# Performance work log

Measured on AMD Instinct MI355X. Metric: run time of the kernel, lower is better.

## Reference

```python
import jax, jax.numpy as jnp
import numpy as np

NEG_SLOPE = 0.2  # PyG GATv2 leaky_relu slope
LN_EPS = 1e-5


def _layernorm(x, gamma, beta):
    mu = x.mean(-1, keepdims=True)
    var = x.var(-1, keepdims=True)
    return (x - mu) * jax.lax.rsqrt(var + LN_EPS) * gamma + beta


def _gatv2_conv(x, src, dst, eattr, Wl, Wr, We, att, bias, concat):
    """PyG GATv2Conv (eval mode). x:(N,F), src/dst:(E,), eattr:(E,edge_dim), att:(H,C)."""
    N = x.shape[0]
    H, C = att.shape
    xl = (x @ Wl).reshape(N, H, C)   # source transform (messages)
    xr = (x @ Wr).reshape(N, H, C)   # target transform
    e = (eattr @ We).reshape(-1, H, C)
    m = xl[src] + xr[dst] + e                                   # (E,H,C)
    score = jnp.sum(jax.nn.leaky_relu(m, NEG_SLOPE) * att, -1)  # (E,H)
    # segment softmax over incoming edges per destination node
    smax = jax.ops.segment_max(score, dst, num_segments=N)
    ex = jnp.exp(score - smax[dst])
    denom = jax.ops.segment_sum(ex, dst, num_segments=N)
    alpha = ex / (denom[dst] + 1e-16)                           # (E,H)
    out = jax.ops.segment_sum(alpha[:, :, None] * xl[src], dst, num_segments=N)  # (N,H,C)
    out = out.reshape(N, H * C) if concat else out.mean(axis=1)
    return out + bias


def setup_inputs() -> dict:
    key = jax.random.key(0)
    ks = jax.random.split(key, 20)
    N, E = 10000, 320000
    D, HID, HEADS, ED = 256, 128, 4, 4
    HC = HID * HEADS  # 512

    def w(k, fi, fo):
        return jax.random.normal(k, (fi, fo), jnp.float32) / np.sqrt(fi)

    x = jax.random.normal(ks[0], (N, D), jnp.float32)
    edge_index = jax.random.randint(ks[1], (2, E), 0, N, jnp.int64)
    edge_attr = jax.random.normal(ks[2], (E, ED), jnp.float32)
    return {
        "x": x, "edge_index": edge_index, "edge_attr": edge_attr,
        # layer 1: heads=4, concat=True
        "Wl1": w(ks[3], D, HC), "Wr1": w(ks[4], D, HC), "We1": w(ks[5], ED, HC),
        "att1": jax.random.normal(ks[6], (HEADS, HID), jnp.float32) / np.sqrt(HID),
        "b1": jnp.zeros((HC,), jnp.float32),
        "g1": jnp.ones((HC,), jnp.float32), "be1": jnp.zeros((HC,), jnp.float32),
        # layer 2: heads=1, concat=False
        "Wl2": w(ks[7], HC, D), "Wr2": w(ks[8], HC, D), "We2": w(ks[9], ED, D),
        "att2": jax.random.normal(ks[10], (1, D), jnp.float32) / np.sqrt(D),
        "b2": jnp.zeros((D,), jnp.float32),
        "g2": jnp.ones((D,), jnp.float32), "be2": jnp.zeros((D,), jnp.float32),
    }


def reference(x, edge_index, edge_attr,
              Wl1, Wr1, We1, att1, b1, g1, be1,
              Wl2, Wr2, We2, att2, b2, g2, be2):
    N = x.shape[0]
    # PyG default add_self_loops=True with edge_attr fill_value='mean'
    loop = jnp.arange(N, dtype=edge_index.dtype)
    src = jnp.concatenate([edge_index[0], loop])
    dst = jnp.concatenate([edge_index[1], loop])
    ea = jnp.concatenate([edge_attr, jnp.broadcast_to(edge_attr.mean(0), (N, edge_attr.shape[1]))])

    h = _gatv2_conv(x, src, dst, ea, Wl1, Wr1, We1, att1, b1, concat=True)
    h = _layernorm(h, g1, be1)
    h = jax.nn.elu(h)  # dropout is identity in eval mode

    h = _gatv2_conv(h, src, dst, ea, Wl2, Wr2, We2, att2, b2, concat=False)
    h = _layernorm(h, g2, be2)
    return h + x  # residual (in_channels == out_channels)
```

## Files before the change

### kernel.cpp

```cpp
#include <hip/hip_runtime.h>
#include <hip/hip_bf16.h>

#define HC1 512
#define HC2 256
#define D_IN 256

typedef __hip_bfloat16  bf16;
typedef __hip_bfloat162 bf162;
typedef __attribute__((ext_vector_type(8))) short short8;
typedef __attribute__((ext_vector_type(4))) float f32x4;
typedef __attribute__((ext_vector_type(2))) float f32x2;

__device__ __forceinline__ void unpack8p(short8 q, f32x2* xa) {
  union { short8 s; unsigned u[4]; } uu; uu.s = q;
#pragma unroll
  for (int j = 0; j < 4; j++) {
    union { unsigned u; float f; } lo, hi;
    lo.u = uu.u[j] << 16;
    hi.u = uu.u[j] & 0xffff0000u;
    xa[j].x = lo.f; xa[j].y = hi.f;
  }
}
__device__ __forceinline__ void load8p(const float* p, f32x2* d) {
  float4 a = *(const float4*)p, b = *(const float4*)(p + 4);
  d[0].x = a.x; d[0].y = a.y; d[1].x = a.z; d[1].y = a.w;
  d[2].x = b.x; d[2].y = b.y; d[3].x = b.z; d[3].y = b.w;
}

template <int CTRL>
__device__ __forceinline__ float dppadd(float x) {
  union { float f; int i; } u, v;
  u.f = x;
  v.i = __builtin_amdgcn_update_dpp(0, u.i, CTRL, 0xF, 0xF, true);
  return x + v.f;
}
__device__ __forceinline__ float red16(float p) {
  p = dppadd<0xB1>(p);
  p = dppadd<0x4E>(p);
  p = dppadd<0x124>(p);
  p = dppadd<0x128>(p);
  return p;
}

__device__ __forceinline__ void glds16(const bf16* g, bf16* l) {
#if __has_builtin(__builtin_amdgcn_global_load_lds)
  __builtin_amdgcn_global_load_lds(
      (const __attribute__((address_space(1))) void*)g,
      (__attribute__((address_space(3))) void*)l, 16, 0, 0);
#else
  int lane = threadIdx.x & 63;
  ((int4*)l)[lane] = *(const int4*)g;
#endif
}

__global__ __launch_bounds__(256)
void gemm_mfma_kernel(const bf16* __restrict__ A, const bf16* __restrict__ BT,
                      bf16* __restrict__ C, int M, int K, int N) {
  __shared__ bf16 lds[8192];
  const int t = threadIdx.x;
  const int w  = t >> 6, l = t & 63;
  const int wr = w >> 1, wc = w & 1;
  const int lo = l & 15, hi = l >> 4;
  const int m0 = blockIdx.y * 128;
  const int n0 = blockIdx.x * 128;

  f32x4 acc[4][4] = {};

  const int c0 = w * 2, c1 = w * 2 + 1;
  const int kc0 = c0 >> 1, r0 = (c0 & 1) * 64 + l;
  const int kc1 = c1 >> 1, r1 = (c1 & 1) * 64 + l;
  int mr0 = m0 + r0; if (mr0 >= M) mr0 = M - 1;
  int mr1 = m0 + r1; if (mr1 >= M) mr1 = M - 1;
  const bf16* ga0 = A + (size_t)mr0 * K + kc0 * 8;
  const bf16* ga1 = A + (size_t)mr1 * K + kc1 * 8;
  const bf16* gb0 = BT + (size_t)(n0 + r0) * K + kc0 * 8;
  const bf16* gb1 = BT + (size_t)(n0 + r1) * K + kc1 * 8;
  bf16* la0 = &lds[c0 * 512];
  bf16* la1 = &lds[c1 * 512];
  bf16* lb0 = &lds[4096 + c0 * 512];
  bf16* lb1 = &lds[4096 + c1 * 512];

  for (int k0 = 0; k0 < K; k0 += 32) {
    if (k0) __syncthreads();
    glds16(ga0 + k0, la0);
    glds16(ga1 + k0, la1);
    glds16(gb0 + k0, lb0);
    glds16(gb1 + k0, lb1);
    __syncthreads();

    short8 af[4], bfr[4];
#pragma unroll
    for (int f = 0; f < 4; f++) {
      af[f]  = *(const short8*)&lds[hi * 1024 + (wr * 64 + f * 16 + lo) * 8];
      bfr[f] = *(const short8*)&lds[4096 + hi * 1024 + (wc * 64 + f * 16 + lo) * 8];
    }
#pragma unroll
    for (int fm = 0; fm < 4; fm++)
#pragma unroll
      for (int fn = 0; fn < 4; fn++)
        acc[fm][fn] = __builtin_amdgcn_mfma_f32_16x16x32_bf16(af[fm], bfr[fn],
                                                              acc[fm][fn], 0, 0, 0);
  }

#pragma unroll
  for (int fm = 0; fm < 4; fm++) {
#pragma unroll
    for (int r = 0; r < 4; r++) {
      int row = m0 + wr * 64 + fm * 16 + hi * 4 + r;
      if (row < M) {
#pragma unroll
        for (int fn = 0; fn < 4; fn++) {
          int col = n0 + wc * 64 + fn * 16 + lo;
          C[(size_t)row * N + col] = __float2bfloat16(acc[fm][fn][r]);
        }
      }
    }
  }
}

__global__ void convx_kernel(const float* __restrict__ x, bf16* __restrict__ xb, int n4) {
  int i = blockIdx.x * blockDim.x + threadIdx.x;
  if (i >= n4) return;
  float4 v = ((const float4*)x)[i];
  union { bf16 h[4]; uint2 u; } cv;
  cv.h[0] = __float2bfloat16(v.x); cv.h[1] = __float2bfloat16(v.y);
  cv.h[2] = __float2bfloat16(v.z); cv.h[3] = __float2bfloat16(v.w);
  ((uint2*)xb)[i] = cv.u;
}

__global__ __launch_bounds__(256)
void transw_kernel(const float* __restrict__ Wl1, const float* __restrict__ Wr1,
                   const float* __restrict__ Wl2, const float* __restrict__ Wr2,
                   bf16* __restrict__ W1T, bf16* __restrict__ W2T) {
  __shared__ float tile[32][33];
  const int z = blockIdx.z;
  const float* in; bf16* out; int K, Nn;
  if (z == 0)      { in = Wl1; out = W1T;             K = 256; Nn = 512; }
  else if (z == 1) { in = Wr1; out = W1T + 512 * 256; K = 256; Nn = 512; }
  else if (z == 2) { in = Wl2; out = W2T;             K = 512; Nn = 256; }
  else             { in = Wr2; out = W2T + 256 * 512; K = 512; Nn = 256; }
  const int nt = blockIdx.x * 32, kt = blockIdx.y * 32;
  if (nt >= Nn || kt >= K) return;
  const int tx = threadIdx.x & 31, ty = threadIdx.x >> 5;
#pragma unroll
  for (int j = 0; j < 4; j++)
    tile[ty + j * 8][tx] = in[(size_t)(kt + ty + j * 8) * Nn + nt + tx];
  __syncthreads();
#pragma unroll
  for (int j = 0; j < 4; j++)
    out[(size_t)(nt + ty + j * 8) * K + kt + tx] = __float2bfloat16(tile[tx][ty + j * 8]);
}

__global__ void mean_kernel(const float* __restrict__ eattr, float* __restrict__ sums, int E) {
  int tid = blockIdx.x * blockDim.x + threadIdx.x;
  int stride = gridDim.x * blockDim.x;
  float l0 = 0.f, l1 = 0.f, l2 = 0.f, l3 = 0.f;
  for (int e = tid; e < E; e += stride) {
    float4 v = ((const float4*)eattr)[e];
    l0 += v.x; l1 += v.y; l2 += v.z; l3 += v.w;
  }
#pragma unroll
  for (int o = 1; o < 64; o <<= 1) {
    l0 += __shfl_xor(l0, o); l1 += __shfl_xor(l1, o);
    l2 += __shfl_xor(l2, o); l3 += __shfl_xor(l3, o);
  }
  if ((threadIdx.x & 63) == 0) {
    atomicAdd(&sums[0], l0); atomicAdd(&sums[1], l1);
    atomicAdd(&sums[2], l2); atomicAdd(&sums[3], l3);
  }
}

__global__ void meanw_kernel(const float* __restrict__ sums, float* __restrict__ mean4, float invE) {
  int t = threadIdx.x;
  if (t < 4) mean4[t] = sums[t] * invE;
}

__global__ void count_kernel(const int* __restrict__ ei, int* __restrict__ counts, int E, int Etot) {
  int tid = blockIdx.x * blockDim.x + threadIdx.x;
  int stride = gridDim.x * blockDim.x;
  for (int e = tid; e < Etot; e += stride) {
    int dst = (e < E) ? ei[E + e] : (e - E);
    atomicAdd(&counts[dst], 1);
  }
}

__global__ __launch_bounds__(1024)
void scan_kernel(const int* __restrict__ counts, int* __restrict__ offs, int N) {
  __shared__ int wsum[16];
  int tid = threadIdx.x, wid = tid >> 6, lane = tid & 63;
  if (tid == 0) offs[0] = 0;
  int carry = 0;
  for (int base = 0; base < N; base += 1024) {
    int i = base + tid;
    int v = (i < N) ? counts[i] : 0;
    int s = v;
#pragma unroll
    for (int o = 1; o < 64; o <<= 1) {
      int u = __shfl_up(s, o);
      if (lane >= o) s += u;
    }
    if (lane == 63) wsum[wid] = s;
    __syncthreads();
    if (wid == 0) {
      int t2 = (lane < 16) ? wsum[lane] : 0;
#pragma unroll
      for (int o = 1; o < 16; o <<= 1) {
        int u = __shfl_up(t2, o);
        if (lane >= o) t2 += u;
      }
      if (lane < 16) wsum[lane] = t2;
    }
    __syncthreads();
    int pre = (wid > 0) ? wsum[wid - 1] : 0;
    int tot = wsum[15];
    if (i < N) offs[i + 1] = carry + pre + s;
    carry += tot;
    __syncthreads();
  }
}

__global__ void fill_kernel(const int* __restrict__ ei, const int* __restrict__ offs,
                            int* __restrict__ cursor, const float* __restrict__ eattr,
                            const float* __restrict__ mean4, int* __restrict__ srcs,
                            float4* __restrict__ eaC, int E, int Etot) {
  int tid = blockIdx.x * blockDim.x + threadIdx.x;
  int stride = gridDim.x * blockDim.x;
  for (int e = tid; e < Etot; e += stride) {
    int src, dst;
    if (e < E) { src = ei[e]; dst = ei[E + e]; } else { src = e - E; dst = src; }
    int pos = atomicAdd(&cursor[dst], 1);
    int slot = offs[dst] + pos;
    srcs[slot] = src;
    eaC[slot] = (e < E) ? ((const float4*)eattr)[e] : *(const float4*)mean4;
  }
}

__global__ __launch_bounds__(256, 3)
void fused1_kernel(const int* __restrict__ srcs, const float4* __restrict__ eaC,
                   const int* __restrict__ offs, const bf16* __restrict__ xlr,
                   const float* __restrict__ We, const float* __restrict__ att,
                   const float* __restrict__ bias, const float* __restrict__ g,
                   const float* __restrict__ be, bf16* __restrict__ h1) {
  const int v = blockIdx.x;
  const int tid = threadIdx.x;
  const int wave = tid >> 6, lane = tid & 63;
  const int ch = lane * 8;

  f32x2 w0p[4], w1p[4], w2p[4], w3p[4], awp[4], xrp[4];
  load8p(We + 0 * HC1 + ch, w0p);
  load8p(We + 1 * HC1 + ch, w1p);
  load8p(We + 2 * HC1 + ch, w2p);
  load8p(We + 3 * HC1 + ch, w3p);
  load8p(att + ch, awp);
  unpack8p(*(const short8*)(xlr + (size_t)v * 1024 + 512 + ch), xrp);

  const int beg = offs[v], end = offs[v + 1];
  const int len = end - beg;
  const int chunk = (len + 3) >> 2;
  int ib = beg + wave * chunk;
  int ie = ib + chunk;
  if (ib > end) ib = end;
  if (ie > end) ie = end;

  float den = 0.f;
  f32x2 accp[4] = {};

  auto edge = [&](short8 q, float4 e) {
    f32x2 xa[4]; unpack8p(q, xa);
    f32x2 p2 = {0.f, 0.f};
#pragma unroll
    for (int j = 0; j < 4; j++) {
      f32x2 m = xa[j] + xrp[j];
      m += e.x * w0p[j];
      m += e.y * w1p[j];
      m += e.z * w2p[j];
      m += e.w * w3p[j];
      f32x2 lm = __builtin_elementwise_max(m, m * 0.2f);
      p2 += lm * awp[j];
    }
    float p = p2.x + p2.y;
    p = red16(p);
    float ex = __expf(p);
    den += ex;
#pragma unroll
    for (int j = 0; j < 4; j++) accp[j] += xa[j] * ex;
  };

  int i = ib;
  if (i + 4 <= ie) {
    int s0 = srcs[i], s1 = srcs[i + 1], s2 = srcs[i + 2], s3 = srcs[i + 3];
    float4 e0 = eaC[i], e1 = eaC[i + 1], e2 = eaC[i + 2], e3 = eaC[i + 3];
    short8 q0 = *(const short8*)(xlr + (size_t)s0 * 1024 + ch);
    short8 q1 = *(const short8*)(xlr + (size_t)s1 * 1024 + ch);
    short8 q2 = *(const short8*)(xlr + (size_t)s2 * 1024 + ch);
    short8 q3 = *(const short8*)(xlr + (size_t)s3 * 1024 + ch);
    i += 4;
    for (; i + 4 <= ie; i += 4) {
      int t0 = srcs[i], t1 = srcs[i + 1], t2 = srcs[i + 2], t3 = srcs[i + 3];
      short8 r0 = *(const short8*)(xlr + (size_t)t0 * 1024 + ch);
      short8 r1 = *(const short8*)(xlr + (size_t)t1 * 1024 + ch);
      short8 r2 = *(const short8*)(xlr + (size_t)t2 * 1024 + ch);
      short8 r3 = *(const short8*)(xlr + (size_t)t3 * 1024 + ch);
      edge(q0, e0); edge(q1, e1); edge(q2, e2); edge(q3, e3);
      e0 = eaC[i]; e1 = eaC[i + 1]; e2 = eaC[i + 2]; e3 = eaC[i + 3];
      q0 = r0; q1 = r1; q2 = r2; q3 = r3;
    }
    edge(q0, e0); edge(q1, e1); edge(q2, e2); edge(q3, e3);
  }
  for (; i < ie; ++i) {
    int s0 = srcs[i];
    float4 e0 = eaC[i];
    short8 q0 = *(const short8*)(xlr + (size_t)s0 * 1024 + ch);
    edge(q0, e0);
  }

  __shared__ float accs[4][HC1];
  __shared__ float dens[4][4];
  __shared__ float2 red[4];
  *(float4*)&accs[wave][ch]     = *(float4*)&accp[0];
  *(float4*)&accs[wave][ch + 4] = *(float4*)&accp[2];
  if ((lane & 15) == 0) dens[wave][lane >> 4] = den;
  __syncthreads();

  const int c = tid * 2;
  const int head = c >> 7;
  const float dtot = dens[0][head] + dens[1][head] + dens[2][head] + dens[3][head];
  const float rden = 1.f / (dtot + 1e-16f);
  float2 a0 = *(float2*)&accs[0][c];
  float2 a1 = *(float2*)&accs[1][c];
  float2 a2 = *(float2*)&accs[2][c];
  float2 a3 = *(float2*)&accs[3][c];
  float2 bv = *(const float2*)(bias + c);
  float val0 = (a0.x + a1.x + a2.x + a3.x) * rden + bv.x;
  float val1 = (a0.y + a1.y + a2.y + a3.y) * rden + bv.y;

  float s1 = val0 + val1, s2 = val0 * val0 + val1 * val1;
  s1 = red16(s1); s2 = red16(s2);
  s1 += __shfl_xor(s1, 16); s2 += __shfl_xor(s2, 16);
  s1 += __shfl_xor(s1, 32); s2 += __shfl_xor(s2, 32);
  if (lane == 0) red[wave] = make_float2(s1, s2);
  __syncthreads();
  float ts1 = red[0].x + red[1].x + red[2].x + red[3].x;
  float ts2 = red[0].y + red[1].y + red[2].y + red[3].y;
  float mu  = ts1 * (1.f / HC1);
  float var = ts2 * (1.f / HC1) - mu * mu;
  float rs  = rsqrtf(var + 1e-5f);

  float2 gv = *(const float2*)(g + c);
  float2 ev = *(const float2*)(be + c);
  float ya = (val0 - mu) * rs * gv.x + ev.x;
  float yb = (val1 - mu) * rs * gv.y + ev.y;
  ya = (ya > 0.f) ? ya : expm1f(ya);
  yb = (yb > 0.f) ? yb : expm1f(yb);
  bf162 hv;
  hv.x = __float2bfloat16(ya); hv.y = __float2bfloat16(yb);
  *(bf162*)(h1 + (size_t)v * HC1 + c) = hv;
}

__global__ __launch_bounds__(256, 3)
void fused2_kernel(const int* __restrict__ srcs, const float4* __restrict__ eaC,
                   const int* __restrict__ offs, const bf16* __restrict__ xlr,
                   const float* __restrict__ We, const float* __restrict__ att,
                   const float* __restrict__ bias, const float* __restrict__ g,
                   const float* __restrict__ be, const float* __restrict__ xin,
                   float* __restrict__ out) {
  const int v = blockIdx.x;
  const int tid = threadIdx.x;
  const int wave = tid >> 6, lane = tid & 63;
  const int half = lane >> 5;
  const int hl = lane & 31;
  const int c0 = hl * 8;

  f32x2 w0p[4], w1p[4], w2p[4], w3p[4], atp[4], xrp[4];
  load8p(We + 0 * HC2 + c0, w0p);
  load8p(We + 1 * HC2 + c0, w1p);
  load8p(We + 2 * HC2 + c0, w2p);
  load8p(We + 3 * HC2 + c0, w3p);
  load8p(att + c0, atp);
  unpack8p(*(const short8*)(xlr + (size_t)v * 512 + 256 + c0), xrp);

  const int beg = offs[v], end = offs[v + 1];
  const int len = end - beg;
  const int chunk = (len + 3) >> 2;
  int ib = beg + wave * chunk;
  int ie = ib + chunk;
  if (ib > end) ib = end;
  if (ie > end) ie = end;

  float den = 0.f;
  f32x2 accp[4] = {};

  auto pair = [&](short8 q, float4 e, bool bvalid) {
    f32x2 xa[4]; unpack8p(q, xa);
    f32x2 p2 = {0.f, 0.f};
#pragma unroll
    for (int j = 0; j < 4; j++) {
      f32x2 m = xa[j] + xrp[j];
      m += e.x * w0p[j];
      m += e.y * w1p[j];
      m += e.z * w2p[j];
      m += e.w * w3p[j];
      f32x2 lm = __builtin_elementwise_max(m, m * 0.2f);
      p2 += lm * atp[j];
    }
    float p = p2.x + p2.y;
    p = red16(p);
    p += __shfl_xor(p, 16);
    float ex = __expf(p);
    if (half && !bvalid) ex = 0.f;
    den += ex;
#pragma unroll
    for (int j = 0; j < 4; j++) accp[j] += xa[j] * ex;
  };

  int i = ib;
  if (i + 4 <= ie) {
    int sA = srcs[i + half],     sB = srcs[i + 2 + half];
    float4 eA = eaC[i + half],   eB = eaC[i + 2 + half];
    short8 qA = *(const short8*)(xlr + (size_t)sA * 512 + c0);
    short8 qB = *(const short8*)(xlr + (size_t)sB * 512 + c0);
    i += 4;
    for (; i + 4 <= ie; i += 4) {
      int tA = srcs[i + half], tB = srcs[i + 2 + half];
      short8 rA = *(const short8*)(xlr + (size_t)tA * 512 + c0);
      short8 rB = *(const short8*)(xlr + (size_t)tB * 512 + c0);
      pair(qA, eA, true); pair(qB, eB, true);
      eA = eaC[i + half]; eB = eaC[i + 2 + half];
      qA = rA; qB = rB;
    }
    pair(qA, eA, true); pair(qB, eB, true);
  }
  for (; i < ie; i += 2) {
    bool hasB = (i + 1 < ie);
    int idx = i + half; if (idx > ie - 1) idx = i;
    int s = srcs[idx];
    float4 e = eaC[idx];
    short8 q = *(const short8*)(xlr + (size_t)s * 512 + c0);
    pair(q, e, hasB);
  }

#pragma unroll
  for (int j = 0; j < 4; j++) {
    accp[j].x += __shfl_xor(accp[j].x, 32);
    accp[j].y += __shfl_xor(accp[j].y, 32);
  }
  den += __shfl_xor(den, 32);

  __shared__ float accs[4][HC2];
  __shared__ float dens[4];
  __shared__ float2 red[4];
  if (half == 0) {
    *(float4*)&accs[wave][c0]     = *(float4*)&accp[0];
    *(float4*)&accs[wave][c0 + 4] = *(float4*)&accp[2];
  }
  if (lane == 0) dens[wave] = den;
  __syncthreads();

  const int c = tid;
  const float dtot = dens[0] + dens[1] + dens[2] + dens[3];
  const float rden = 1.f / (dtot + 1e-16f);
  float val = (accs[0][c] + accs[1][c] + accs[2][c] + accs[3][c]) * rden + bias[c];

  float s1 = val, s2 = val * val;
  s1 = red16(s1); s2 = red16(s2);
  s1 += __shfl_xor(s1, 16); s2 += __shfl_xor(s2, 16);
  s1 += __shfl_xor(s1, 32); s2 += __shfl_xor(s2, 32);
  if (lane == 0) red[wave] = make_float2(s1, s2);
  __syncthreads();
  float ts1 = red[0].x + red[1].x + red[2].x + red[3].x;
  float ts2 = red[0].y + red[1].y + red[2].y + red[3].y;
  float mu  = ts1 * (1.f / HC2);
  float var = ts2 * (1.f / HC2) - mu * mu;
  float rs  = rsqrtf(var + 1e-5f);
  float y = (val - mu) * rs * g[c] + be[c];
  out[(size_t)v * HC2 + c] = y + xin[(size_t)v * HC2 + c];
}

extern "C" void kernel_launch(void* const* d_in, const int* in_sizes, int n_in,
                              void* d_out, int out_size, void* d_ws, size_t ws_size,
                              hipStream_t stream) {
  const float* x     = (const float*)d_in[0];
  const int*   ei    = (const int*)d_in[1];
  const float* eattr = (const float*)d_in[2];
  const float* Wl1   = (const float*)d_in[3];
  const float* Wr1   = (const float*)d_in[4];
  const float* We1   = (const float*)d_in[5];
  const float* att1  = (const float*)d_in[6];
  const float* b1    = (const float*)d_in[7];
  const float* g1    = (const float*)d_in[8];
  const float* be1   = (const float*)d_in[9];
  const float* Wl2   = (const float*)d_in[10];
  const float* Wr2   = (const float*)d_in[11];
  const float* We2   = (const float*)d_in[12];
  const float* att2  = (const float*)d_in[13];
  const float* b2    = (const float*)d_in[14];
  const float* g2    = (const float*)d_in[15];
  const float* be2   = (const float*)d_in[16];

  const int N    = in_sizes[0] / D_IN;
  const int E    = in_sizes[2] / 4;
  const int Etot = E + N;

  char* w = (char*)d_ws;
  auto alloc = [&](size_t bytes) -> void* {
    void* p = (void*)w;
    w += (bytes + 255) & ~(size_t)255;
    return p;
  };
  bf16*   xb    = (bf16*)alloc((size_t)N * D_IN * 2);
  bf16*   W1T   = (bf16*)alloc((size_t)1024 * 256 * 2);
  bf16*   W2T   = (bf16*)alloc((size_t)512 * 512 * 2);
  bf16*   xlr1  = (bf16*)alloc((size_t)N * 1024 * 2);
  bf16*   h1    = (bf16*)alloc((size_t)N * HC1 * 2);
  bf16*   xlr2  = (bf16*)alloc((size_t)N * 512 * 2);
  int*    srcs  = (int*)alloc((size_t)Etot * 4);
  float4* eaC   = (float4*)alloc((size_t)Etot * 16);
  int*    offs  = (int*)alloc((size_t)(N + 1) * 4);
  float*  mean4 = (float*)alloc(64);
  char*   zb    = w;
  int*    counts = (int*)alloc((size_t)N * 4);
  int*    cursor = (int*)alloc((size_t)N * 4);
  float*  sums   = (float*)alloc(64);
  size_t  zbytes = (size_t)(w - zb);

  hipMemsetAsync(zb, 0, zbytes, stream);

  int n4 = N * D_IN / 4;
  convx_kernel<<<(n4 + 255) / 256, 256, 0, stream>>>(x, xb, n4);
  transw_kernel<<<dim3(16, 16, 4), 256, 0, stream>>>(Wl1, Wr1, Wl2, Wr2, W1T, W2T);

  mean_kernel<<<256, 256, 0, stream>>>(eattr, sums, E);
  meanw_kernel<<<1, 64, 0, stream>>>(sums, mean4, 1.f / (float)E);

  count_kernel<<<1024, 256, 0, stream>>>(ei, counts, E, Etot);
  scan_kernel<<<1, 1024, 0, stream>>>(counts, offs, N);
  fill_kernel<<<1024, 256, 0, stream>>>(ei, offs, cursor, eattr, mean4, srcs, eaC, E, Etot);

  dim3 gg1(1024 / 128, (N + 127) / 128);
  gemm_mfma_kernel<<<gg1, 256, 0, stream>>>(xb, W1T, xlr1, N, 256, 1024);

  fused1_kernel<<<N, 256, 0, stream>>>(srcs, eaC, offs, xlr1, We1, att1, b1, g1, be1, h1);

  dim3 gg2(512 / 128, (N + 127) / 128);
  gemm_mfma_kernel<<<gg2, 256, 0, stream>>>(h1, W2T, xlr2, N, 512, 512);

  fused2_kernel<<<N, 256, 0, stream>>>(srcs, eaC, offs, xlr2, We2, att2,
                                       b2, g2, be2, x, (float*)d_out);
}
```

Before: 287.9 us.

## Merge preprocessing kernels, drop software prefetch in edge loops, raise occupancy

Folds the edge-attribute mean reduction into the dst-count kernel and moves the mean normalisation into the scan kernel, removing two launches. The fused attention kernels lose their register-held next-iteration prefetch, so each batch of four edges is loaded and then processed. Launch bounds for fused1 go from 3 to 4 blocks per SM so more waves can hide gather latency. This trades explicit load/compute overlap for lower register pressure and higher occupancy, and it adds an unused unpack4p helper.

```diff
diff --git a/kernel.cpp b/kernel.cpp
--- a/kernel.cpp
+++ b/kernel.cpp
@@ -15,6 +15,16 @@
   union { short8 s; unsigned u[4]; } uu; uu.s = q;
 #pragma unroll
   for (int j = 0; j < 4; j++) {
+    union { unsigned u; float f; } lo, hi;
+    lo.u = uu.u[j] << 16;
+    hi.u = uu.u[j] & 0xffff0000u;
+    xa[j].x = lo.f; xa[j].y = hi.f;
+  }
+}
+__device__ __forceinline__ void unpack4p(short4 qs, f32x2* xa) {
+  union { short4 s; unsigned u[2]; } uu; uu.s = qs;
+#pragma unroll
+  for (int j = 0; j < 2; j++) {
     union { unsigned u; float f; } lo, hi;
     lo.u = uu.u[j] << 16;
     hi.u = uu.u[j] & 0xffff0000u;
@@ -151,13 +161,19 @@
     out[(size_t)(nt + ty + j * 8) * K + kt + tx] = __float2bfloat16(tile[tx][ty + j * 8]);
 }
 
-__global__ void mean_kernel(const float* __restrict__ eattr, float* __restrict__ sums, int E) {
+__global__ void count_mean_kernel(const int* __restrict__ ei, const float* __restrict__ eattr,
+                                  int* __restrict__ counts, float* __restrict__ sums,
+                                  int E, int Etot) {
   int tid = blockIdx.x * blockDim.x + threadIdx.x;
   int stride = gridDim.x * blockDim.x;
   float l0 = 0.f, l1 = 0.f, l2 = 0.f, l3 = 0.f;
-  for (int e = tid; e < E; e += stride) {
-    float4 v = ((const float4*)eattr)[e];
-    l0 += v.x; l1 += v.y; l2 += v.z; l3 += v.w;
+  for (int e = tid; e < Etot; e += stride) {
+    int dst = (e < E) ? ei[E + e] : (e - E);
+    atomicAdd(&counts[dst], 1);
+    if (e < E) {
+      float4 v = ((const float4*)eattr)[e];
+      l0 += v.x; l1 += v.y; l2 += v.z; l3 += v.w;
+    }
   }
 #pragma unroll
   for (int o = 1; o < 64; o <<= 1) {
@@ -170,24 +186,13 @@
   }
 }
 
-__global__ void meanw_kernel(const float* __restrict__ sums, float* __restrict__ mean4, float invE) {
-  int t = threadIdx.x;
-  if (t < 4) mean4[t] = sums[t] * invE;
-}
-
-__global__ void count_kernel(const int* __restrict__ ei, int* __restrict__ counts, int E, int Etot) {
-  int tid = blockIdx.x * blockDim.x + threadIdx.x;
-  int stride = gridDim.x * blockDim.x;
-  for (int e = tid; e < Etot; e += stride) {
-    int dst = (e < E) ? ei[E + e] : (e - E);
-    atomicAdd(&counts[dst], 1);
-  }
-}
-
 __global__ __launch_bounds__(1024)
-void scan_kernel(const int* __restrict__ counts, int* __restrict__ offs, int N) {
+void scan_kernel(const int* __restrict__ counts, int* __restrict__ offs,
+                 const float* __restrict__ sums, float* __restrict__ mean4,
+                 float invE, int N) {
   __shared__ int wsum[16];
   int tid = threadIdx.x, wid = tid >> 6, lane = tid & 63;
+  if (tid < 4) mean4[tid] = sums[tid] * invE;
   if (tid == 0) offs[0] = 0;
   int carry = 0;
   for (int base = 0; base < N; base += 1024) {
@@ -235,7 +240,7 @@
   }
 }
 
-__global__ __launch_bounds__(256, 3)
+__global__ __launch_bounds__(256, 4)
 void fused1_kernel(const int* __restrict__ srcs, const float4* __restrict__ eaC,
                    const int* __restrict__ offs, const bf16* __restrict__ xlr,
                    const float* __restrict__ We, const float* __restrict__ att,
@@ -287,24 +292,13 @@
   };
 
   int i = ib;
-  if (i + 4 <= ie) {
+  for (; i + 4 <= ie; i += 4) {
     int s0 = srcs[i], s1 = srcs[i + 1], s2 = srcs[i + 2], s3 = srcs[i + 3];
     float4 e0 = eaC[i], e1 = eaC[i + 1], e2 = eaC[i + 2], e3 = eaC[i + 3];
     short8 q0 = *(const short8*)(xlr + (size_t)s0 * 1024 + ch);
     short8 q1 = *(const short8*)(xlr + (size_t)s1 * 1024 + ch);
     short8 q2 = *(const short8*)(xlr + (size_t)s2 * 1024 + ch);
     short8 q3 = *(const short8*)(xlr + (size_t)s3 * 1024 + ch);
-    i += 4;
-    for (; i + 4 <= ie; i += 4) {
-      int t0 = srcs[i], t1 = srcs[i + 1], t2 = srcs[i + 2], t3 = srcs[i + 3];
-      short8 r0 = *(const short8*)(xlr + (size_t)t0 * 1024 + ch);
-      short8 r1 = *(const short8*)(xlr + (size_t)t1 * 1024 + ch);
-      short8 r2 = *(const short8*)(xlr + (size_t)t2 * 1024 + ch);
-      short8 r3 = *(const short8*)(xlr + (size_t)t3 * 1024 + ch);
-      edge(q0, e0); edge(q1, e1); edge(q2, e2); edge(q3, e3);
-      e0 = eaC[i]; e1 = eaC[i + 1]; e2 = eaC[i + 2]; e3 = eaC[i + 3];
-      q0 = r0; q1 = r1; q2 = r2; q3 = r3;
-    }
     edge(q0, e0); edge(q1, e1); edge(q2, e2); edge(q3, e3);
   }
   for (; i < ie; ++i) {
@@ -414,20 +408,11 @@
   };
 
   int i = ib;
-  if (i + 4 <= ie) {
-    int sA = srcs[i + half],     sB = srcs[i + 2 + half];
-    float4 eA = eaC[i + half],   eB = eaC[i + 2 + half];
+  for (; i + 4 <= ie; i += 4) {
+    int sA = srcs[i + half],   sB = srcs[i + 2 + half];
+    float4 eA = eaC[i + half], eB = eaC[i + 2 + half];
     short8 qA = *(const short8*)(xlr + (size_t)sA * 512 + c0);
     short8 qB = *(const short8*)(xlr + (size_t)sB * 512 + c0);
-    i += 4;
-    for (; i + 4 <= ie; i += 4) {
-      int tA = srcs[i + half], tB = srcs[i + 2 + half];
-      short8 rA = *(const short8*)(xlr + (size_t)tA * 512 + c0);
-      short8 rB = *(const short8*)(xlr + (size_t)tB * 512 + c0);
-      pair(qA, eA, true); pair(qB, eB, true);
-      eA = eaC[i + half]; eB = eaC[i + 2 + half];
-      qA = rA; qB = rB;
-    }
     pair(qA, eA, true); pair(qB, eB, true);
   }
   for (; i < ie; i += 2) {
@@ -529,11 +514,8 @@
   convx_kernel<<<(n4 + 255) / 256, 256, 0, stream>>>(x, xb, n4);
   transw_kernel<<<dim3(16, 16, 4), 256, 0, stream>>>(Wl1, Wr1, Wl2, Wr2, W1T, W2T);
 
-  mean_kernel<<<256, 256, 0, stream>>>(eattr, sums, E);
-  meanw_kernel<<<1, 64, 0, stream>>>(sums, mean4, 1.f / (float)E);
-
-  count_kernel<<<1024, 256, 0, stream>>>(ei, counts, E, Etot);
-  scan_kernel<<<1, 1024, 0, stream>>>(counts, offs, N);
+  count_mean_kernel<<<1024, 256, 0, stream>>>(ei, eattr, counts, sums, E, Etot);
+  scan_kernel<<<1, 1024, 0, stream>>>(counts, offs, sums, mean4, 1.f / (float)E, N);
   fill_kernel<<<1024, 256, 0, stream>>>(ei, offs, cursor, eattr, mean4, srcs, eaC, E, Etot);
 
   dim3 gg1(1024 / 128, (N + 127) / 128);
```

After: 421.0 us. +46.2%, slower.
